# Kernel tuning notes

Measured on AMD Instinct MI355X. Metric: run time of the kernel, lower is better.

## Reference

```python
import jax, jax.numpy as jnp
import numpy as np

# LIF constants from __init__ defaults and forward body
TAU = 20.0        # membrane time constant
TH = 1.0          # base threshold
TAU_ADAPT = 100.0 # adaptation time constant
BETA_ADAPT = 1.5  # adaptation strength
V_RESET = -0.5    # reset potential
K = 10.0          # surrogate sigmoid slope


def setup_inputs() -> dict:
    key = jax.random.key(0)
    I = jax.random.normal(key, (16384, 2048), dtype=jnp.float32)
    return {"I": I}


def reference(I):
    # I: (B, L). Sequential LIF recurrence over L via lax.scan.
    B, L = I.shape
    dtype = I.dtype

    def step(carry, I_t):
        v, a, s_num = carry  # each (B,)
        th_eff = TH + BETA_ADAPT * a
        v = v - v / TAU + I_t  # v += dv
        s_soft = jax.nn.sigmoid(K * (v - th_eff))
        s_hard = (v >= th_eff).astype(dtype)
        # straight-through: forward value = s_hard, grad flows via s_soft
        s = jax.lax.stop_gradient(s_hard - s_soft) + s_soft
        s_num = s_num + s
        s_det = jax.lax.stop_gradient(s)  # reset is non-differentiable (detached)
        v = v * (1.0 - s_det) + V_RESET * s_det
        a = a - a / TAU_ADAPT + s
        return (v, a, s_num), (s, s_num)

    zeros = jnp.zeros((B,), dtype)
    _, (spikes_t, series_t) = jax.lax.scan(step, (zeros, zeros, zeros), I.T)
    # scan outputs are (L, B); transpose back to (B, L)
    return spikes_t.T, series_t.T
```

## Files before the change

kernel.cpp:

```cpp
#include <hip/hip_runtime.h>


#define LIF_L  2048
#define TILE   64
#define NTILES (LIF_L / TILE)

constexpr float kR20 = -0.5f / 20.0f;
constexpr float kC0  = -0.5f - kR20;

__device__ __forceinline__ void barrier_lds_only() {
    asm volatile("s_waitcnt lgkmcnt(0)\n\ts_barrier" ::: "memory");
}

__device__ __forceinline__ float lif_step(float Inext, float& vn, float& a, float& th) {
    bool fire = (vn >= th);
    float s = fire ? 1.0f : 0.0f;
    float q0 = __fmul_rn(vn, 0.05f);
    float r  = __fmaf_rn(-20.0f, q0, vn);
    float d  = __fmaf_rn(r, 0.05f, q0);
    float ns = __fadd_rn(__fsub_rn(vn, d), Inext);
    float ss = __fadd_rn(kC0, Inext);
    vn = fire ? ss : ns;
    float qa = __fmul_rn(a, 0.01f);
    float ra = __fmaf_rn(-100.0f, qa, a);
    float da = __fmaf_rn(ra, 0.01f, qa);
    float ap  = __fsub_rn(a, da);
    float ap1 = __fadd_rn(ap, 1.0f);
    a = fire ? ap1 : ap;
    th = __fadd_rn(1.0f, __fmul_rn(1.5f, a));
    return s;
}

__device__ __forceinline__ int sw_idx(int row, int g) {
    return row * 64 + (((g) ^ (row & 15)) << 2);
}

__global__ __launch_bounds__(128, 1) void lif_fwd(const float* __restrict__ I,
                                                  float* __restrict__ spikes,
                                                  float* __restrict__ series) {
    __shared__ float sp_tile[4][64 * 64];
    __shared__ float se_tile[64 * 64];

    const int tid  = threadIdx.x;
    const int wave = tid >> 6;
    const int lane = tid & 63;
    const int row0 = blockIdx.x * 64;

    const float4* __restrict__ I4 =
        reinterpret_cast<const float4*>(I + (size_t)(row0 + lane) * LIF_L);

    float vn = 0.0f, a = 0.0f, th = 1.0f;
    float4 bufA[16], bufB[16];
    float carry = 0.0f;

    if (wave == 0) {
        #pragma unroll
        for (int i = 0; i < 16; ++i) bufA[i] = I4[i];
        #pragma unroll
        for (int i = 0; i < 16; ++i) bufB[i] = I4[16 + i];
    }

    auto compute_tile = [&](const float4* buf, float nx0, float* sp) {
        #pragma unroll
        for (int c = 0; c < 16; ++c) {
            float4 in = buf[c];
            float nxt = (c < 15) ? buf[c + 1].x : nx0;
            float4 os;
            os.x = lif_step(in.y, vn, a, th);
            os.y = lif_step(in.z, vn, a, th);
            os.z = lif_step(in.w, vn, a, th);
            os.w = lif_step(nxt,  vn, a, th);
            *reinterpret_cast<float4*>(&sp[sw_idx(lane, c)]) = os;
        }
    };

    auto helper_tile = [&](int tkt, const float* sp) {
        #pragma unroll
        for (int c = 0; c < 16; ++c) {
            int ix = sw_idx(lane, c);
            float4 sv = *reinterpret_cast<const float4*>(&sp[ix]);
            float4 nv;
            carry = __fadd_rn(carry, sv.x); nv.x = carry;
            carry = __fadd_rn(carry, sv.y); nv.y = carry;
            carry = __fadd_rn(carry, sv.z); nv.z = carry;
            carry = __fadd_rn(carry, sv.w); nv.w = carry;
            *reinterpret_cast<float4*>(&se_tile[ix]) = nv;
        }
        const size_t colbase = (size_t)tkt * TILE;
        #pragma unroll
        for (int i = 0; i < 16; ++i) {
            int row = i * 4 + (lane >> 4);
            int g   = lane & 15;
            int ix  = sw_idx(row, g);
            float4 vs = *reinterpret_cast<const float4*>(&sp[ix]);
            float4 ve = *reinterpret_cast<const float4*>(&se_tile[ix]);
            size_t gaddr = (size_t)(row0 + row) * LIF_L + colbase + (size_t)g * 4;
            *reinterpret_cast<float4*>(spikes + gaddr) = vs;
            *reinterpret_cast<float4*>(series + gaddr) = ve;
        }
    };

    if (wave == 0) vn = bufA[0].x;

    for (int p = 0; p < NTILES / 2; ++p) {
        const int kt = 2 * p;
        if (wave == 0) {
            compute_tile(bufA, bufB[0].x, sp_tile[kt & 3]);
            if (kt + 2 < NTILES) {
                #pragma unroll
                for (int i = 0; i < 16; ++i) bufA[i] = I4[(kt + 2) * 16 + i];
            }
            float nx0 = (kt + 2 < NTILES) ? bufA[0].x : 0.0f;
            compute_tile(bufB, nx0, sp_tile[(kt + 1) & 3]);
            if (kt + 3 < NTILES) {
                #pragma unroll
                for (int i = 0; i < 16; ++i) bufB[i] = I4[(kt + 3) * 16 + i];
            }
        } else if (p > 0) {
            helper_tile(kt - 2, sp_tile[(kt - 2) & 3]);
            helper_tile(kt - 1, sp_tile[(kt - 1) & 3]);
        }
        barrier_lds_only();
    }
    if (wave == 1) {
        helper_tile(NTILES - 2, sp_tile[(NTILES - 2) & 3]);
        helper_tile(NTILES - 1, sp_tile[(NTILES - 1) & 3]);
    }
}

extern "C" void kernel_launch(void* const* d_in, const int* in_sizes, int n_in,
                              void* d_out, int out_size, void* d_ws, size_t ws_size,
                              hipStream_t stream) {
    const float* I = (const float*)d_in[0];
    const int B = in_sizes[0] / LIF_L;
    float* spikes = (float*)d_out;
    float* series = (float*)d_out + (size_t)B * LIF_L;

    const int threads = 128;
    const int blocks = B / 64;
    lif_fwd<<<blocks, threads, 0, stream>>>(I, spikes, series);
}
```

Baseline: 377.2 us.

## Fold spike prefix sum into compute wave and split flush across two helper waves

The running spike count is now accumulated inside the recurrence step and written to a per-tile LDS buffer, so the helper waves only copy spike and series tiles to global memory. A third wave is added so the two tiles of each pair are flushed in parallel by separate waves. The step also selects the pre-input term before adding the input and adds the spike directly to the adaptation variable, shortening the dependent chain. This costs more LDS (four series buffers) and extra LDS stores in the latency-critical compute wave.

New measurement: 383.9 us. Within noise of the previous version (+1.8%).

```diff
diff --git a/kernel.cpp b/kernel.cpp
--- a/kernel.cpp
+++ b/kernel.cpp
@@ -12,21 +12,22 @@
     asm volatile("s_waitcnt lgkmcnt(0)\n\ts_barrier" ::: "memory");
 }
 
-__device__ __forceinline__ float lif_step(float Inext, float& vn, float& a, float& th) {
+__device__ __forceinline__ float lif_step(float Inext, float& vn, float& a,
+                                          float& th, float& carry) {
     bool fire = (vn >= th);
     float s = fire ? 1.0f : 0.0f;
     float q0 = __fmul_rn(vn, 0.05f);
     float r  = __fmaf_rn(-20.0f, q0, vn);
     float d  = __fmaf_rn(r, 0.05f, q0);
-    float ns = __fadd_rn(__fsub_rn(vn, d), Inext);
-    float ss = __fadd_rn(kC0, Inext);
-    vn = fire ? ss : ns;
+    float dec = __fsub_rn(vn, d);
+    float sel = fire ? kC0 : dec;
+    vn = __fadd_rn(sel, Inext);
+    carry = __fadd_rn(carry, s);
     float qa = __fmul_rn(a, 0.01f);
     float ra = __fmaf_rn(-100.0f, qa, a);
     float da = __fmaf_rn(ra, 0.01f, qa);
-    float ap  = __fsub_rn(a, da);
-    float ap1 = __fadd_rn(ap, 1.0f);
-    a = fire ? ap1 : ap;
+    float ap = __fsub_rn(a, da);
+    a = __fadd_rn(ap, s);
     th = __fadd_rn(1.0f, __fmul_rn(1.5f, a));
     return s;
 }
@@ -35,11 +36,11 @@
     return row * 64 + (((g) ^ (row & 15)) << 2);
 }
 
-__global__ __launch_bounds__(128, 1) void lif_fwd(const float* __restrict__ I,
+__global__ __launch_bounds__(192, 1) void lif_fwd(const float* __restrict__ I,
                                                   float* __restrict__ spikes,
                                                   float* __restrict__ series) {
     __shared__ float sp_tile[4][64 * 64];
-    __shared__ float se_tile[64 * 64];
+    __shared__ float se_tile[4][64 * 64];
 
     const int tid  = threadIdx.x;
     const int wave = tid >> 6;
@@ -49,9 +50,8 @@
     const float4* __restrict__ I4 =
         reinterpret_cast<const float4*>(I + (size_t)(row0 + lane) * LIF_L);
 
-    float vn = 0.0f, a = 0.0f, th = 1.0f;
+    float vn = 0.0f, a = 0.0f, th = 1.0f, carry = 0.0f;
     float4 bufA[16], bufB[16];
-    float carry = 0.0f;
 
     if (wave == 0) {
         #pragma unroll
@@ -60,32 +60,22 @@
         for (int i = 0; i < 16; ++i) bufB[i] = I4[16 + i];
     }
 
-    auto compute_tile = [&](const float4* buf, float nx0, float* sp) {
+    auto compute_tile = [&](const float4* buf, float nx0, float* sp, float* se) {
         #pragma unroll
         for (int c = 0; c < 16; ++c) {
             float4 in = buf[c];
             float nxt = (c < 15) ? buf[c + 1].x : nx0;
-            float4 os;
-            os.x = lif_step(in.y, vn, a, th);
-            os.y = lif_step(in.z, vn, a, th);
-            os.z = lif_step(in.w, vn, a, th);
-            os.w = lif_step(nxt,  vn, a, th);
+            float4 os, oc;
+            os.x = lif_step(in.y, vn, a, th, carry); oc.x = carry;
+            os.y = lif_step(in.z, vn, a, th, carry); oc.y = carry;
+            os.z = lif_step(in.w, vn, a, th, carry); oc.z = carry;
+            os.w = lif_step(nxt,  vn, a, th, carry); oc.w = carry;
             *reinterpret_cast<float4*>(&sp[sw_idx(lane, c)]) = os;
+            *reinterpret_cast<float4*>(&se[sw_idx(lane, c)]) = oc;
         }
     };
 
-    auto helper_tile = [&](int tkt, const float* sp) {
-        #pragma unroll
-        for (int c = 0; c < 16; ++c) {
-            int ix = sw_idx(lane, c);
-            float4 sv = *reinterpret_cast<const float4*>(&sp[ix]);
-            float4 nv;
-            carry = __fadd_rn(carry, sv.x); nv.x = carry;
-            carry = __fadd_rn(carry, sv.y); nv.y = carry;
-            carry = __fadd_rn(carry, sv.z); nv.z = carry;
-            carry = __fadd_rn(carry, sv.w); nv.w = carry;
-            *reinterpret_cast<float4*>(&se_tile[ix]) = nv;
-        }
+    auto flush_tile = [&](int tkt, const float* sp, const float* se) {
         const size_t colbase = (size_t)tkt * TILE;
         #pragma unroll
         for (int i = 0; i < 16; ++i) {
@@ -93,7 +83,7 @@
             int g   = lane & 15;
             int ix  = sw_idx(row, g);
             float4 vs = *reinterpret_cast<const float4*>(&sp[ix]);
-            float4 ve = *reinterpret_cast<const float4*>(&se_tile[ix]);
+            float4 ve = *reinterpret_cast<const float4*>(&se[ix]);
             size_t gaddr = (size_t)(row0 + row) * LIF_L + colbase + (size_t)g * 4;
             *reinterpret_cast<float4*>(spikes + gaddr) = vs;
             *reinterpret_cast<float4*>(series + gaddr) = ve;
@@ -105,26 +95,30 @@
     for (int p = 0; p < NTILES / 2; ++p) {
         const int kt = 2 * p;
         if (wave == 0) {
-            compute_tile(bufA, bufB[0].x, sp_tile[kt & 3]);
+            compute_tile(bufA, bufB[0].x, sp_tile[kt & 3], se_tile[kt & 3]);
             if (kt + 2 < NTILES) {
                 #pragma unroll
                 for (int i = 0; i < 16; ++i) bufA[i] = I4[(kt + 2) * 16 + i];
             }
             float nx0 = (kt + 2 < NTILES) ? bufA[0].x : 0.0f;
-            compute_tile(bufB, nx0, sp_tile[(kt + 1) & 3]);
+            compute_tile(bufB, nx0, sp_tile[(kt + 1) & 3], se_tile[(kt + 1) & 3]);
             if (kt + 3 < NTILES) {
                 #pragma unroll
                 for (int i = 0; i < 16; ++i) bufB[i] = I4[(kt + 3) * 16 + i];
             }
         } else if (p > 0) {
-            helper_tile(kt - 2, sp_tile[(kt - 2) & 3]);
-            helper_tile(kt - 1, sp_tile[(kt - 1) & 3]);
+            if (wave == 1) {
+                flush_tile(kt - 2, sp_tile[(kt - 2) & 3], se_tile[(kt - 2) & 3]);
+            } else {
+                flush_tile(kt - 1, sp_tile[(kt - 1) & 3], se_tile[(kt - 1) & 3]);
+            }
         }
         barrier_lds_only();
     }
     if (wave == 1) {
-        helper_tile(NTILES - 2, sp_tile[(NTILES - 2) & 3]);
-        helper_tile(NTILES - 1, sp_tile[(NTILES - 1) & 3]);
+        flush_tile(NTILES - 2, sp_tile[(NTILES - 2) & 3], se_tile[(NTILES - 2) & 3]);
+    } else if (wave == 2) {
+        flush_tile(NTILES - 1, sp_tile[(NTILES - 1) & 3], se_tile[(NTILES - 1) & 3]);
     }
 }
 
@@ -136,7 +130,7 @@
     float* spikes = (float*)d_out;
     float* series = (float*)d_out + (size_t)B * LIF_L;
 
-    const int threads = 128;
+    const int threads = 192;
     const int blocks = B / 64;
     lif_fwd<<<blocks, threads, 0, stream>>>(I, spikes, series);
 }
```
